# Optimization experiments

Measured on AMD Instinct MI355X. Metric: run time of the kernel, lower is better.

Reference implementation:

```python
import jax, jax.numpy as jnp
import numpy as np

N_NODES = 50000
N_EDGES = 500000
ATOM_DIM = 128
BOND_DIM = 64
EMB = 128
N_GRAPHS = 256
NUM_LAYER = 2


def _kaiming_uniform(key, fan_out, fan_in):
    # kaiming_uniform_ with nonlinearity='relu': bound = sqrt(6 / fan_in) * sqrt(2)/1 adjustments
    gain = np.sqrt(2.0)
    bound = gain * np.sqrt(3.0 / fan_in)
    return jax.random.uniform(key, (fan_out, fan_in), jnp.float32, -bound, bound)


def setup_inputs() -> dict:
    key = jax.random.key(0)
    ks = jax.random.split(key, 12)
    x = jax.random.normal(ks[0], (N_NODES, ATOM_DIM), jnp.float32)
    edge_attr = jax.random.normal(ks[1], (N_EDGES, BOND_DIM), jnp.float32)
    edge_index = jax.random.randint(ks[2], (2, N_EDGES), 0, N_NODES, jnp.int64)
    batch = jnp.sort(jax.random.randint(ks[3], (N_NODES,), 0, N_GRAPHS, jnp.int64))
    Wa = _kaiming_uniform(ks[4], EMB, ATOM_DIM)
    ba = jnp.zeros((EMB,), jnp.float32)
    Wb = _kaiming_uniform(ks[5], EMB, BOND_DIM)
    bb = jnp.zeros((EMB,), jnp.float32)
    W1 = _kaiming_uniform(ks[6], EMB, EMB)
    b1 = jnp.zeros((EMB,), jnp.float32)
    W2 = _kaiming_uniform(ks[7], EMB // 2, EMB)
    b2 = jnp.zeros((EMB // 2,), jnp.float32)
    W3 = _kaiming_uniform(ks[8], 1, EMB // 2)
    return {"x": x, "edge_attr": edge_attr, "edge_index": edge_index, "batch": batch,
            "Wa": Wa, "ba": ba, "Wb": Wb, "bb": bb,
            "W1": W1, "b1": b1, "W2": W2, "b2": b2, "W3": W3}


def reference(x, edge_attr, edge_index, batch, Wa, ba, Wb, bb, W1, b1, W2, b2, W3):
    src, dst = edge_index[0], edge_index[1]
    # Step 1: embeddings
    node_emb = x @ Wa.T + ba          # [N, EMB]
    edge_emb = edge_attr @ Wb.T + bb  # [E, EMB]
    # Step 2: message passing layers: gather, multiply with edge_emb, scatter-add, residual
    for _ in range(NUM_LAYER):
        msg = node_emb[src] * edge_emb                           # [E, EMB]
        agg = jax.ops.segment_sum(msg, dst, num_segments=N_NODES)  # [N, EMB]
        node_emb = node_emb + agg
    # Step 3: energy MLP (ReLU first, per nn.Sequential)
    h = jax.nn.relu(node_emb)
    h = jax.nn.relu(h @ W1.T + b1)
    h = jax.nn.relu(h @ W2.T + b2)
    node_energy = h @ W3.T            # [N, 1], no bias
    # Step 4: global add pool over graphs
    dg = jax.ops.segment_sum(node_energy, batch, num_segments=N_GRAPHS)  # [G, 1]
    return dg
```

## Files before the change

### kernel.cpp

```cpp
#include <hip/hip_runtime.h>
#include <cstdio>
#include <cstdint>

#define N_NODES 50000
#define N_EDGES 500000
#define EMB 128
#define BOND 64
#define NGRAPH 256
#define NB_SCAN ((N_NODES + 255) / 256)
#define NSTRIP (N_NODES / 16)
#define ESTRIP (N_EDGES / 16)

typedef short bf16x8 __attribute__((ext_vector_type(8)));
typedef float f32x4  __attribute__((ext_vector_type(4)));

__device__ __forceinline__ unsigned short f2bf(float v){
  unsigned u = __float_as_uint(v);
  unsigned r = (u + 0x7fffu + ((u >> 16) & 1u)) >> 16;
  return (unsigned short)r;
}
__device__ __forceinline__ float bf2f(unsigned short u){
  return __uint_as_float(((unsigned)u) << 16);
}
__device__ __forceinline__ unsigned short brelu(unsigned short u){
  return (u & 0x8000u) ? (unsigned short)0 : u;
}


__global__ void prep_w(const float* __restrict__ Wa, const float* __restrict__ W1,
                       const float* __restrict__ W2, const float* __restrict__ Wb,
                       unsigned short* __restrict__ wabf, unsigned short* __restrict__ w1bf,
                       unsigned short* __restrict__ w2bf, unsigned short* __restrict__ wbbf)
{
  int i = blockIdx.x * 256 + threadIdx.x;
  if (i < 40960){
    int i2 = i & 16383;
    int j = i2 & 7, lb = (i2 >> 3) & 63, kc = (i2 >> 9) & 3, tn = i2 >> 11;
    int lm = lb & 15, q = lb >> 4;
    int row = tn * 16 + lm, col = kc * 32 + q * 8 + j;
    if (i < 16384){
      wabf[i] = f2bf(Wa[row * EMB + col]);
    } else if (i < 32768){
      int pcol = j * 16 + kc * 4 + q;
      w1bf[i2] = f2bf(W1[row * EMB + pcol]);
    } else {
      w2bf[i2] = f2bf(W2[row * EMB + col]);
    }
  } else if (i < 49152){
    int i2 = i - 40960;
    int j = i2 & 7, l = (i2 >> 3) & 63, kc = (i2 >> 9) & 1, tn = i2 >> 10;
    int lm = l & 15, q = l >> 4;
    wbbf[i2] = f2bf(Wb[(tn * 16 + lm) * BOND + kc * 32 + q * 8 + j]);
  }
}

__global__ __launch_bounds__(256) void node_gemm_mfma(const float* __restrict__ x,
    const unsigned short* __restrict__ wabf, const float* __restrict__ ba,
    unsigned short* __restrict__ out)
{
  const int t = threadIdx.x;
  const int wv = t >> 6, l = t & 63;
  const int lm = l & 15, q = l >> 4;
  union U8 { bf16x8 v; unsigned short s[8]; };
  const int strip = blockIdx.x * 4 + wv;
  if (strip >= NSTRIP) return;
  const long n0 = (long)strip * 16;

  bf16x8 a[4];
  #pragma unroll
  for (int kc = 0; kc < 4; kc++){
    const float* ap = x + (n0 + lm) * (long)EMB + kc * 32 + q * 8;
    float4 x0 = *(const float4*)ap;
    float4 x1 = *(const float4*)(ap + 4);
    U8 u;
    u.s[0] = f2bf(x0.x); u.s[1] = f2bf(x0.y); u.s[2] = f2bf(x0.z); u.s[3] = f2bf(x0.w);
    u.s[4] = f2bf(x1.x); u.s[5] = f2bf(x1.y); u.s[6] = f2bf(x1.z); u.s[7] = f2bf(x1.w);
    a[kc] = u.v;
  }
  float biasv[8];
  #pragma unroll
  for (int tn = 0; tn < 8; tn++) biasv[tn] = ba[tn * 16 + lm];

  f32x4 acc[8];
  #pragma unroll
  for (int tn = 0; tn < 8; tn++) acc[tn] = (f32x4){0.f, 0.f, 0.f, 0.f};
  #pragma unroll
  for (int kc = 0; kc < 4; kc++){
    #pragma unroll
    for (int tn = 0; tn < 8; tn++){
      bf16x8 bf = *(const bf16x8*)(wabf + (size_t)((tn * 4 + kc) * 64 + l) * 8);
      acc[tn] = __builtin_amdgcn_mfma_f32_16x16x32_bf16(a[kc], bf, acc[tn], 0, 0, 0);
    }
  }
  #pragma unroll
  for (int i = 0; i < 4; i++){
    U8 o;
    #pragma unroll
    for (int tn = 0; tn < 8; tn++) o.s[tn] = f2bf(acc[tn][i] + biasv[tn]);
    *(bf16x8*)(out + (n0 + q * 4 + i) * (long)EMB + lm * 8) = o.v;
  }
}

__global__ __launch_bounds__(256) void edge_gemm_mfma(
    const float* __restrict__ attr, const unsigned short* __restrict__ wbbf,
    const float* __restrict__ bb, const int* __restrict__ pos,
    unsigned short* __restrict__ eemb)
{
  const int t = threadIdx.x;
  const int l = t & 63;
  const int lm = l & 15, q = l >> 4;
  union U8 { bf16x8 v; unsigned short s[8]; };

  bf16x8 bfrag[8][2];
  float bias[8];
  #pragma unroll
  for (int tn = 0; tn < 8; tn++){
    bias[tn] = bb[tn * 16 + lm];
    #pragma unroll
    for (int kc = 0; kc < 2; kc++)
      bfrag[tn][kc] = *(const bf16x8*)(wbbf + (size_t)((tn * 2 + kc) * 64 + l) * 8);
  }

  const long wid = (long)blockIdx.x * 4 + (t >> 6);
  const long stride = (long)gridDim.x * 4 * 16;
  for (long e0 = wid * 16; e0 < N_EDGES; e0 += stride){
    int4 pv = *(const int4*)(pos + e0 + q * 4);
    bf16x8 af[2];
    #pragma unroll
    for (int kc = 0; kc < 2; kc++){
      const float* ap = attr + (e0 + lm) * (long)BOND + kc * 32 + q * 8;
      float4 a0 = *(const float4*)ap;
      float4 a1 = *(const float4*)(ap + 4);
      U8 u;
      u.s[0] = f2bf(a0.x); u.s[1] = f2bf(a0.y); u.s[2] = f2bf(a0.z); u.s[3] = f2bf(a0.w);
      u.s[4] = f2bf(a1.x); u.s[5] = f2bf(a1.y); u.s[6] = f2bf(a1.z); u.s[7] = f2bf(a1.w);
      af[kc] = u.v;
    }
    f32x4 acc[8];
    #pragma unroll
    for (int tn = 0; tn < 8; tn++) acc[tn] = (f32x4){0.f, 0.f, 0.f, 0.f};
    #pragma unroll
    for (int kc = 0; kc < 2; kc++){
      #pragma unroll
      for (int tn = 0; tn < 8; tn++)
        acc[tn] = __builtin_amdgcn_mfma_f32_16x16x32_bf16(af[kc], bfrag[tn][kc], acc[tn], 0, 0, 0);
    }
    int pr[4] = {pv.x, pv.y, pv.z, pv.w};
    #pragma unroll
    for (int i = 0; i < 4; i++){
      U8 o;
      #pragma unroll
      for (int tn = 0; tn < 8; tn++) o.s[tn] = f2bf(acc[tn][i] + bias[tn]);
      *(bf16x8*)(eemb + (long)pr[i] * EMB + lm * 8) = o.v;
    }
  }
}


__global__ __launch_bounds__(256) void count_deg(const int* __restrict__ ei,
                                                 int* __restrict__ deg)
{
  int e = blockIdx.x * 256 + threadIdx.x;
  if (e < N_EDGES) atomicAdd(&deg[ei[N_EDGES + e]], 1);
}

__global__ __launch_bounds__(256) void scan_s1(const int* __restrict__ deg,
                                               int* __restrict__ blocksum)
{
  int i = blockIdx.x * 256 + threadIdx.x;
  int lane = threadIdx.x & 63, w = threadIdx.x >> 6;
  int v = (i < N_NODES) ? deg[i] : 0;
  #pragma unroll
  for (int o = 32; o > 0; o >>= 1) v += __shfl_down(v, o, 64);
  __shared__ int ws4[4];
  if (lane == 0) ws4[w] = v;
  __syncthreads();
  if (threadIdx.x == 0) blocksum[blockIdx.x] = ws4[0] + ws4[1] + ws4[2] + ws4[3];
}

__global__ __launch_bounds__(256) void scan_s2(const int* __restrict__ blocksum,
                                               int* __restrict__ blockoff,
                                               int* __restrict__ off)
{
  int t = threadIdx.x;
  int lane = t & 63, w = t >> 6;
  int v = (t < NB_SCAN) ? blocksum[t] : 0;
  int x = v;
  #pragma unroll
  for (int d = 1; d < 64; d <<= 1){
    int y = __shfl_up(x, d, 64);
    if (lane >= d) x += y;
  }
  __shared__ int wsum[4];
  if (lane == 63) wsum[w] = x;
  __syncthreads();
  int wo = 0;
  for (int j = 0; j < w; j++) wo += wsum[j];
  if (t < NB_SCAN) blockoff[t] = wo + x - v;
  if (t == 0) off[N_NODES] = wsum[0] + wsum[1] + wsum[2] + wsum[3];
}

__global__ __launch_bounds__(256) void scan_s3(const int* __restrict__ deg,
    const int* __restrict__ blockoff, int* __restrict__ off, int* __restrict__ fill)
{
  int i = blockIdx.x * 256 + threadIdx.x;
  int lane = threadIdx.x & 63, w = threadIdx.x >> 6;
  int v = (i < N_NODES) ? deg[i] : 0;
  int x = v;
  #pragma unroll
  for (int d = 1; d < 64; d <<= 1){
    int y = __shfl_up(x, d, 64);
    if (lane >= d) x += y;
  }
  __shared__ int wsum[4];
  if (lane == 63) wsum[w] = x;
  __syncthreads();
  int wo = 0;
  for (int j = 0; j < w; j++) wo += wsum[j];
  if (i < N_NODES){
    int excl = blockoff[blockIdx.x] + wo + x - v;
    off[i] = excl;
    fill[i] = excl;
  }
}

__global__ __launch_bounds__(256) void scatter_edges(const int* __restrict__ ei,
    int* __restrict__ fill, int2* __restrict__ cse, int* __restrict__ pos)
{
  int e = blockIdx.x * 256 + threadIdx.x;
  if (e < N_EDGES){
    int dst = ei[N_EDGES + e];
    int p = atomicAdd(&fill[dst], 1);
    cse[p] = make_int2(ei[e], e);
    pos[e] = p;
  }
}

__global__ __launch_bounds__(256) void agg_kernel(const unsigned short* __restrict__ node_old,
    const unsigned short* __restrict__ eemb, const int* __restrict__ off,
    const int2* __restrict__ cse, unsigned short* __restrict__ node_new)
{
  int n = blockIdx.x * 8 + (threadIdx.x >> 5);
  if (n >= N_NODES) return;
  int c0 = (threadIdx.x & 31) * 4;
  int s = off[n], e = off[n + 1];
  ushort4 r = *(const ushort4*)(node_old + (long)n * EMB + c0);
  float4 accA = make_float4(bf2f(r.x), bf2f(r.y), bf2f(r.z), bf2f(r.w));
  float4 accB = make_float4(0.f, 0.f, 0.f, 0.f);
  int i = s;

#define AGG_BLOCK(CNT)                                                        \
  {                                                                           \
    int idx[CNT];                                                             \
    _Pragma("unroll")                                                         \
    for (int j = 0; j < CNT; j++) idx[j] = cse[i + j].x;                      \
    ushort4 a[CNT], eb[CNT];                                                  \
    _Pragma("unroll")                                                         \
    for (int j = 0; j < CNT; j++){                                            \
      a[j]  = *(const ushort4*)(node_old + (long)idx[j] * EMB + c0);          \
      eb[j] = *(const ushort4*)(eemb + (long)(i + j) * EMB + c0);             \
    }                                                                         \
    _Pragma("unroll")                                                         \
    for (int j = 0; j < CNT; j++){                                            \
      float4& acc = (j & 1) ? accB : accA;                                    \
      acc.x = fmaf(bf2f(a[j].x), bf2f(eb[j].x), acc.x);                       \
      acc.y = fmaf(bf2f(a[j].y), bf2f(eb[j].y), acc.y);                       \
      acc.z = fmaf(bf2f(a[j].z), bf2f(eb[j].z), acc.z);                       \
      acc.w = fmaf(bf2f(a[j].w), bf2f(eb[j].w), acc.w);                       \
    }                                                                         \
    i += CNT;                                                                 \
  }

  for (; i + 8 <= e; ) AGG_BLOCK(8)
  if (i + 4 <= e) AGG_BLOCK(4)
  if (i + 2 <= e) AGG_BLOCK(2)
  if (i < e) AGG_BLOCK(1)
#undef AGG_BLOCK

  ushort4 o;
  o.x = f2bf(accA.x + accB.x);
  o.y = f2bf(accA.y + accB.y);
  o.z = f2bf(accA.z + accB.z);
  o.w = f2bf(accA.w + accB.w);
  *(ushort4*)(node_new + (long)n * EMB + c0) = o;
}

__global__ __launch_bounds__(256) void mlp_mfma_pool(const unsigned short* __restrict__ ne,
    const unsigned short* __restrict__ w1bf, const unsigned short* __restrict__ w2bf,
    const float* __restrict__ b1, const float* __restrict__ b2,
    const float* __restrict__ W3, const int* __restrict__ batch,
    float* __restrict__ dg)
{
  __shared__ float h1s[4][16 * 132];
  __shared__ float pool[NGRAPH];
  const int t = threadIdx.x;
  const int wv = t >> 6, l = t & 63;
  const int lm = l & 15, q = l >> 4;
  union U8 { bf16x8 v; unsigned short s[8]; };

  for (int i = t; i < NGRAPH; i += 256) pool[i] = 0.f;
  __syncthreads();

  const int strip = blockIdx.x * 4 + wv;
  if (strip < NSTRIP){
    const long n0 = (long)strip * 16;

    float b1v[8], b2v[4], w3v[4];
    #pragma unroll
    for (int tn = 0; tn < 8; tn++) b1v[tn] = b1[tn * 16 + lm];
    #pragma unroll
    for (int tc = 0; tc < 4; tc++){ b2v[tc] = b2[tc * 16 + lm]; w3v[tc] = W3[tc * 16 + lm]; }

    bf16x8 a1[4];
    #pragma unroll
    for (int kc = 0; kc < 4; kc++){
      const unsigned short* ap = ne + (n0 + lm) * (long)EMB + kc * 32 + q * 8;
      ushort4 v0 = *(const ushort4*)ap;
      ushort4 v1 = *(const ushort4*)(ap + 4);
      U8 u;
      u.s[0] = brelu(v0.x); u.s[1] = brelu(v0.y); u.s[2] = brelu(v0.z); u.s[3] = brelu(v0.w);
      u.s[4] = brelu(v1.x); u.s[5] = brelu(v1.y); u.s[6] = brelu(v1.z); u.s[7] = brelu(v1.w);
      a1[kc] = u.v;
    }

    f32x4 acc1[8];
    #pragma unroll
    for (int tn = 0; tn < 8; tn++) acc1[tn] = (f32x4){b1v[tn], b1v[tn], b1v[tn], b1v[tn]};
    #pragma unroll
    for (int kc = 0; kc < 4; kc++){
      #pragma unroll
      for (int tn = 0; tn < 8; tn++){
        bf16x8 bf = *(const bf16x8*)(w1bf + (size_t)((tn * 4 + kc) * 64 + l) * 8);
        acc1[tn] = __builtin_amdgcn_mfma_f32_16x16x32_bf16(a1[kc], bf, acc1[tn], 0, 0, 0);
      }
    }

    float* h1 = h1s[wv];
    #pragma unroll
    for (int tn = 0; tn < 8; tn++)
      #pragma unroll
      for (int i = 0; i < 4; i++)
        h1[(q * 4 + i) * 132 + tn * 16 + lm] = fmaxf(acc1[tn][i], 0.f);
    bf16x8 a2[4];
    #pragma unroll
    for (int kc = 0; kc < 4; kc++){
      const float* hp = h1 + lm * 132 + kc * 32 + q * 8;
      float4 x0 = *(const float4*)hp;
      float4 x1 = *(const float4*)(hp + 4);
      U8 u;
      u.s[0] = f2bf(x0.x); u.s[1] = f2bf(x0.y); u.s[2] = f2bf(x0.z); u.s[3] = f2bf(x0.w);
      u.s[4] = f2bf(x1.x); u.s[5] = f2bf(x1.y); u.s[6] = f2bf(x1.z); u.s[7] = f2bf(x1.w);
      a2[kc] = u.v;
    }

    f32x4 acc2[4];
    #pragma unroll
    for (int tc = 0; tc < 4; tc++) acc2[tc] = (f32x4){b2v[tc], b2v[tc], b2v[tc], b2v[tc]};
    #pragma unroll
    for (int kc = 0; kc < 4; kc++){
      #pragma unroll
      for (int tc = 0; tc < 4; tc++){
        bf16x8 bf = *(const bf16x8*)(w2bf + (size_t)((tc * 4 + kc) * 64 + l) * 8);
        acc2[tc] = __builtin_amdgcn_mfma_f32_16x16x32_bf16(a2[kc], bf, acc2[tc], 0, 0, 0);
      }
    }

    float e4[4];
    #pragma unroll
    for (int i = 0; i < 4; i++){
      float s = 0.f;
      #pragma unroll
      for (int tc = 0; tc < 4; tc++) s = fmaf(fmaxf(acc2[tc][i], 0.f), w3v[tc], s);
      e4[i] = s;
    }
    #pragma unroll
    for (int m = 1; m < 16; m <<= 1)
      #pragma unroll
      for (int i = 0; i < 4; i++) e4[i] += __shfl_xor(e4[i], m, 64);
    if (lm == 0){
      #pragma unroll
      for (int i = 0; i < 4; i++){
        int node = (int)n0 + q * 4 + i;
        atomicAdd(&pool[batch[node]], e4[i]);
      }
    }
  }
  __syncthreads();
  for (int i = t; i < NGRAPH; i += 256){
    float v = pool[i];
    if (v != 0.f) atomicAdd(&dg[i], v);
  }
}

extern "C" void kernel_launch(void* const* d_in, const int* in_sizes, int n_in,
                              void* d_out, int out_size, void* d_ws, size_t ws_size,
                              hipStream_t stream)
{
  const float* x         = (const float*)d_in[0];
  const float* edge_attr = (const float*)d_in[1];
  const int*   ei        = (const int*)d_in[2];
  const int*   batch     = (const int*)d_in[3];
  const float* Wa = (const float*)d_in[4];
  const float* ba = (const float*)d_in[5];
  const float* Wb = (const float*)d_in[6];
  const float* bb = (const float*)d_in[7];
  const float* W1 = (const float*)d_in[8];
  const float* b1 = (const float*)d_in[9];
  const float* W2 = (const float*)d_in[10];
  const float* b2 = (const float*)d_in[11];
  const float* W3 = (const float*)d_in[12];

  char* ws = (char*)d_ws;
  size_t p = 0;
  auto alloc = [&](size_t bytes) -> char* {
    char* q = ws + p;
    p += (bytes + 255) & ~(size_t)255;
    return q;
  };
  unsigned short* bufA = (unsigned short*)alloc((size_t)N_NODES * EMB * 2);
  unsigned short* bufB = (unsigned short*)alloc((size_t)N_NODES * EMB * 2);
  unsigned short* eemb = (unsigned short*)alloc((size_t)N_EDGES * EMB * 2);
  unsigned short* wabf = (unsigned short*)alloc(16384 * sizeof(short));
  unsigned short* w1bf = (unsigned short*)alloc(16384 * sizeof(short));
  unsigned short* w2bf = (unsigned short*)alloc(8192 * sizeof(short));
  unsigned short* wbbf = (unsigned short*)alloc(8192 * sizeof(short));
  int* deg  = (int*)alloc(N_NODES * sizeof(int));
  int* off  = (int*)alloc((N_NODES + 1) * sizeof(int));
  int* fill = (int*)alloc(N_NODES * sizeof(int));
  int* blocksum = (int*)alloc(NB_SCAN * sizeof(int));
  int* blockoff = (int*)alloc(NB_SCAN * sizeof(int));
  int2* cse = (int2*)alloc((size_t)N_EDGES * sizeof(int2));
  int* pos  = (int*)alloc((size_t)N_EDGES * sizeof(int));
  if (p > ws_size){
    fprintf(stderr, "kernel_launch: ws too small (%zu < %zu)\n", ws_size, p);
    return;
  }

  hipMemsetAsync(deg, 0, N_NODES * sizeof(int), stream);
  count_deg<<<(N_EDGES + 255) / 256, 256, 0, stream>>>(ei, deg);
  scan_s1<<<NB_SCAN, 256, 0, stream>>>(deg, blocksum);
  scan_s2<<<1, 256, 0, stream>>>(blocksum, blockoff, off);
  scan_s3<<<NB_SCAN, 256, 0, stream>>>(deg, blockoff, off, fill);
  scatter_edges<<<(N_EDGES + 255) / 256, 256, 0, stream>>>(ei, fill, cse, pos);

  prep_w<<<192, 256, 0, stream>>>(Wa, W1, W2, Wb, wabf, w1bf, w2bf, wbbf);
  node_gemm_mfma<<<(NSTRIP + 3) / 4, 256, 0, stream>>>(x, wabf, ba, bufA);
  edge_gemm_mfma<<<2048, 256, 0, stream>>>(edge_attr, wbbf, bb, pos, eemb);

  agg_kernel<<<(N_NODES + 7) / 8, 256, 0, stream>>>(bufA, eemb, off, cse, bufB);
  agg_kernel<<<(N_NODES + 7) / 8, 256, 0, stream>>>(bufB, eemb, off, cse, bufA);

  hipMemsetAsync(d_out, 0, NGRAPH * sizeof(float), stream);
  mlp_mfma_pool<<<(NSTRIP + 3) / 4, 256, 0, stream>>>(bufA, w1bf, w2bf, b1, b2, W3, batch, (float*)d_out);
}
```

Baseline: 416.7 us.

## Pre-convert edge attributes to bf16 and gather them in CSR order

Edge attributes are converted to bf16 in a pass fused into the degree-count kernel. The edge GEMM then iterates in CSR (destination-sorted) order, gathering bf16 attribute rows by edge id and writing edge embeddings contiguously. This replaces the scattered 256-byte output writes through the pos array with gathered 128-byte reads, and removes the pos array. The cost is an extra write and read of a bf16 copy of the attributes (64 MB) and a gather on the input side.

```diff
diff --git a/kernel.cpp b/kernel.cpp
--- a/kernel.cpp
+++ b/kernel.cpp
@@ -10,8 +10,10 @@
 #define NB_SCAN ((N_NODES + 255) / 256)
 #define NSTRIP (N_NODES / 16)
 #define ESTRIP (N_EDGES / 16)
+#define NCHUNK (N_EDGES * BOND / 8)
 
 typedef short bf16x8 __attribute__((ext_vector_type(8)));
+typedef unsigned short u16x8 __attribute__((ext_vector_type(8)));
 typedef float f32x4  __attribute__((ext_vector_type(4)));
 
 __device__ __forceinline__ unsigned short f2bf(float v){
@@ -102,8 +104,8 @@
 }
 
 __global__ __launch_bounds__(256) void edge_gemm_mfma(
-    const float* __restrict__ attr, const unsigned short* __restrict__ wbbf,
-    const float* __restrict__ bb, const int* __restrict__ pos,
+    const unsigned short* __restrict__ attr_bf, const unsigned short* __restrict__ wbbf,
+    const float* __restrict__ bb, const int2* __restrict__ cse,
     unsigned short* __restrict__ eemb)
 {
   const int t = threadIdx.x;
@@ -123,45 +125,42 @@
 
   const long wid = (long)blockIdx.x * 4 + (t >> 6);
   const long stride = (long)gridDim.x * 4 * 16;
-  for (long e0 = wid * 16; e0 < N_EDGES; e0 += stride){
-    int4 pv = *(const int4*)(pos + e0 + q * 4);
-    bf16x8 af[2];
-    #pragma unroll
-    for (int kc = 0; kc < 2; kc++){
-      const float* ap = attr + (e0 + lm) * (long)BOND + kc * 32 + q * 8;
-      float4 a0 = *(const float4*)ap;
-      float4 a1 = *(const float4*)(ap + 4);
-      U8 u;
-      u.s[0] = f2bf(a0.x); u.s[1] = f2bf(a0.y); u.s[2] = f2bf(a0.z); u.s[3] = f2bf(a0.w);
-      u.s[4] = f2bf(a1.x); u.s[5] = f2bf(a1.y); u.s[6] = f2bf(a1.z); u.s[7] = f2bf(a1.w);
-      af[kc] = u.v;
-    }
+  for (long p0 = wid * 16; p0 < N_EDGES; p0 += stride){
+    long eid = (long)cse[p0 + lm].y;
+    bf16x8 af0 = *(const bf16x8*)(attr_bf + eid * BOND + q * 8);
+    bf16x8 af1 = *(const bf16x8*)(attr_bf + eid * BOND + 32 + q * 8);
     f32x4 acc[8];
     #pragma unroll
     for (int tn = 0; tn < 8; tn++) acc[tn] = (f32x4){0.f, 0.f, 0.f, 0.f};
     #pragma unroll
-    for (int kc = 0; kc < 2; kc++){
-      #pragma unroll
-      for (int tn = 0; tn < 8; tn++)
-        acc[tn] = __builtin_amdgcn_mfma_f32_16x16x32_bf16(af[kc], bfrag[tn][kc], acc[tn], 0, 0, 0);
-    }
-    int pr[4] = {pv.x, pv.y, pv.z, pv.w};
+    for (int tn = 0; tn < 8; tn++){
+      acc[tn] = __builtin_amdgcn_mfma_f32_16x16x32_bf16(af0, bfrag[tn][0], acc[tn], 0, 0, 0);
+      acc[tn] = __builtin_amdgcn_mfma_f32_16x16x32_bf16(af1, bfrag[tn][1], acc[tn], 0, 0, 0);
+    }
     #pragma unroll
     for (int i = 0; i < 4; i++){
       U8 o;
       #pragma unroll
       for (int tn = 0; tn < 8; tn++) o.s[tn] = f2bf(acc[tn][i] + bias[tn]);
-      *(bf16x8*)(eemb + (long)pr[i] * EMB + lm * 8) = o.v;
-    }
-  }
-}
-
-
-__global__ __launch_bounds__(256) void count_deg(const int* __restrict__ ei,
-                                                 int* __restrict__ deg)
-{
-  int e = blockIdx.x * 256 + threadIdx.x;
-  if (e < N_EDGES) atomicAdd(&deg[ei[N_EDGES + e]], 1);
+      *(bf16x8*)(eemb + (p0 + q * 4 + i) * (long)EMB + lm * 8) = o.v;
+    }
+  }
+}
+
+
+__global__ __launch_bounds__(256) void count_deg_conv(const int* __restrict__ ei,
+    int* __restrict__ deg, const float* __restrict__ attr,
+    unsigned short* __restrict__ attr_bf)
+{
+  int id = blockIdx.x * 256 + threadIdx.x;
+  if (id < N_EDGES) atomicAdd(&deg[ei[N_EDGES + id]], 1);
+  const float* s = attr + (size_t)id * 8;
+  float4 a0 = *(const float4*)s;
+  float4 a1 = *(const float4*)(s + 4);
+  u16x8 o;
+  o[0] = f2bf(a0.x); o[1] = f2bf(a0.y); o[2] = f2bf(a0.z); o[3] = f2bf(a0.w);
+  o[4] = f2bf(a1.x); o[5] = f2bf(a1.y); o[6] = f2bf(a1.z); o[7] = f2bf(a1.w);
+  *(u16x8*)(attr_bf + (size_t)id * 8) = o;
 }
 
 __global__ __launch_bounds__(256) void scan_s1(const int* __restrict__ deg,
@@ -225,14 +224,13 @@
 }
 
 __global__ __launch_bounds__(256) void scatter_edges(const int* __restrict__ ei,
-    int* __restrict__ fill, int2* __restrict__ cse, int* __restrict__ pos)
+    int* __restrict__ fill, int2* __restrict__ cse)
 {
   int e = blockIdx.x * 256 + threadIdx.x;
   if (e < N_EDGES){
     int dst = ei[N_EDGES + e];
     int p = atomicAdd(&fill[dst], 1);
     cse[p] = make_int2(ei[e], e);
-    pos[e] = p;
   }
 }
 
@@ -420,6 +418,7 @@
   unsigned short* bufA = (unsigned short*)alloc((size_t)N_NODES * EMB * 2);
   unsigned short* bufB = (unsigned short*)alloc((size_t)N_NODES * EMB * 2);
   unsigned short* eemb = (unsigned short*)alloc((size_t)N_EDGES * EMB * 2);
+  unsigned short* attr_bf = (unsigned short*)alloc((size_t)N_EDGES * BOND * 2);
   unsigned short* wabf = (unsigned short*)alloc(16384 * sizeof(short));
   unsigned short* w1bf = (unsigned short*)alloc(16384 * sizeof(short));
   unsigned short* w2bf = (unsigned short*)alloc(8192 * sizeof(short));
@@ -430,22 +429,21 @@
   int* blocksum = (int*)alloc(NB_SCAN * sizeof(int));
   int* blockoff = (int*)alloc(NB_SCAN * sizeof(int));
   int2* cse = (int2*)alloc((size_t)N_EDGES * sizeof(int2));
-  int* pos  = (int*)alloc((size_t)N_EDGES * sizeof(int));
   if (p > ws_size){
     fprintf(stderr, "kernel_launch: ws too small (%zu < %zu)\n", ws_size, p);
     return;
   }
 
   hipMemsetAsync(deg, 0, N_NODES * sizeof(int), stream);
-  count_deg<<<(N_EDGES + 255) / 256, 256, 0, stream>>>(ei, deg);
+  count_deg_conv<<<NCHUNK / 256, 256, 0, stream>>>(ei, deg, edge_attr, attr_bf);
   scan_s1<<<NB_SCAN, 256, 0, stream>>>(deg, blocksum);
   scan_s2<<<1, 256, 0, stream>>>(blocksum, blockoff, off);
   scan_s3<<<NB_SCAN, 256, 0, stream>>>(deg, blockoff, off, fill);
-  scatter_edges<<<(N_EDGES + 255) / 256, 256, 0, stream>>>(ei, fill, cse, pos);
+  scatter_edges<<<(N_EDGES + 255) / 256, 256, 0, stream>>>(ei, fill, cse);
 
   prep_w<<<192, 256, 0, stream>>>(Wa, W1, W2, Wb, wabf, w1bf, w2bf, wbbf);
   node_gemm_mfma<<<(NSTRIP + 3) / 4, 256, 0, stream>>>(x, wabf, ba, bufA);
-  edge_gemm_mfma<<<2048, 256, 0, stream>>>(edge_attr, wbbf, bb, pos, eemb);
+  edge_gemm_mfma<<<2048, 256, 0, stream>>>(attr_bf, wbbf, bb, cse, eemb);
 
   agg_kernel<<<(N_NODES + 7) / 8, 256, 0, stream>>>(bufA, eemb, off, cse, bufB);
   agg_kernel<<<(N_NODES + 7) / 8, 256, 0, stream>>>(bufB, eemb, off, cse, bufA);
```

Result: slower. 426.9 us (+2.5%).
